# Kernel tuning notes

Measured on AMD Instinct MI355X. Metric: run time of the kernel, lower is better.

The kernel has to match this reference:

```python
import jax, jax.numpy as jnp
import numpy as np

B, N, E, H = 4, 2048, 512, 8
D = E // H  # head dim = 64


def setup_inputs() -> dict:
    key = jax.random.key(0)
    ks = jax.random.split(key, 5)
    s = 1.0 / np.sqrt(E)
    return {
        "x": jax.random.normal(ks[0], (B, N, E), dtype=jnp.float32),
        "Wk": jax.random.normal(ks[1], (E, E), dtype=jnp.float32) * s,
        "bk": jax.random.normal(ks[2], (E,), dtype=jnp.float32) * s,
        "Wv": jax.random.normal(ks[3], (E, E), dtype=jnp.float32) * s,
        "bv": jax.random.normal(ks[4], (E,), dtype=jnp.float32) * s,
    }


def reference(x, Wk, bk, Wv, bv):
    b, n, e = x.shape
    # Linear projections (torch Linear: y = x @ W.T + b), split into heads.
    keys = (x @ Wk.T + bk).reshape(b, n, H, D).transpose(0, 2, 1, 3)    # b h n d
    values = (x @ Wv.T + bv).reshape(b, n, H, D).transpose(0, 2, 1, 3)  # b h n d
    # Q = K self-attention: scores [b, h, n, n]
    dotprod = jnp.einsum('bhnd,bhmd->bhnm', keys, keys)
    # softmax over last axis, then unusual POST-softmax scaling by sqrt(emb)
    att = jax.nn.softmax(dotprod, axis=-1) / jnp.sqrt(jnp.asarray(e, x.dtype))
    # dropout p=0 -> identity
    out = jnp.einsum('bhnm,bhmd->bhnd', att, values)
    return out.transpose(0, 2, 1, 3).reshape(b, n, e)
```

## Files before the change

kernel.cpp:

```cpp
#include <hip/hip_runtime.h>

typedef __bf16 bf16_t;
typedef bf16_t bf16x8 __attribute__((ext_vector_type(8)));
typedef float f32x4 __attribute__((ext_vector_type(4)));

#define NSEQ 2048
#define EMB 512
#define HEADS 8
#define HD 64
#define BATCH 4
#define LOG2E 1.4426950408889634f

#define MFMA16(a, b, c) __builtin_amdgcn_mfma_f32_16x16x32_bf16(a, b, c, 0, 0, 0)


__global__ __launch_bounds__(256, 2) void proj_kernel(
    const float* __restrict__ x,
    const float* __restrict__ Wk, const float* __restrict__ bk,
    const float* __restrict__ Wv, const float* __restrict__ bv,
    bf16_t* __restrict__ Kf, bf16_t* __restrict__ Vf)
{
  __shared__ union {
    struct {
      __align__(16) bf16_t A[2][128][40];
      __align__(16) bf16_t B[2][128][40];
    } s;
    __align__(16) bf16_t T[128][136];
  } u;

  const int t    = threadIdx.x;
  const int w    = t >> 6;
  const int lane = t & 63;
  const int quad = lane >> 4;
  const int l15  = lane & 15;
  const int wr   = w >> 1, wc = w & 1;
  const int m0   = blockIdx.x * 128;
  const int n0   = blockIdx.y * 128;
  const int zz   = (blockIdx.y >= 4);
  const float* __restrict__ W = zz ? Wv : Wk;
  const int nW = n0 - zz * 512;

  const int sr = t >> 3;
  const int sj = t & 7;
  const int sb = sj >> 2, sc = (sj & 3) * 8;

  float4 pa[4][2], pb[4][2];
  auto prefetch = [&](int k0) {
#pragma unroll
    for (int i = 0; i < 4; ++i) {
      const float* xa = x + (size_t)(m0 + sr + i * 32) * EMB + k0 + sj * 8;
      const float* wa = W + (size_t)(nW + sr + i * 32) * EMB + k0 + sj * 8;
      pa[i][0] = *(const float4*)xa; pa[i][1] = *(const float4*)(xa + 4);
      pb[i][0] = *(const float4*)wa; pb[i][1] = *(const float4*)(wa + 4);
    }
  };
  auto pack8 = [](float4 a, float4 b) -> bf16x8 {
    bf16x8 v;
    v[0] = (bf16_t)a.x; v[1] = (bf16_t)a.y; v[2] = (bf16_t)a.z; v[3] = (bf16_t)a.w;
    v[4] = (bf16_t)b.x; v[5] = (bf16_t)b.y; v[6] = (bf16_t)b.z; v[7] = (bf16_t)b.w;
    return v;
  };

  f32x4 acc[4][4] = {};
  prefetch(0);

  for (int it = 0; it < 8; ++it) {
    __syncthreads();
#pragma unroll
    for (int i = 0; i < 4; ++i) {
      *(bf16x8*)(&u.s.A[sb][sr + i * 32][sc]) = pack8(pa[i][0], pa[i][1]);
      *(bf16x8*)(&u.s.B[sb][sr + i * 32][sc]) = pack8(pb[i][0], pb[i][1]);
    }
    __syncthreads();
    if (it < 7) prefetch((it + 1) * 64);

    bf16x8 af[4][2], bf[4][2];
#pragma unroll
    for (int mt = 0; mt < 4; ++mt)
#pragma unroll
      for (int kk = 0; kk < 2; ++kk)
        af[mt][kk] = *(const bf16x8*)(&u.s.A[kk][wr * 64 + mt * 16 + l15][quad * 8]);
#pragma unroll
    for (int nt = 0; nt < 4; ++nt)
#pragma unroll
      for (int kk = 0; kk < 2; ++kk)
        bf[nt][kk] = *(const bf16x8*)(&u.s.B[kk][wc * 64 + nt * 16 + l15][quad * 8]);
#pragma unroll
    for (int kk = 0; kk < 2; ++kk)
#pragma unroll
      for (int mt = 0; mt < 4; ++mt)
#pragma unroll
        for (int nt = 0; nt < 4; ++nt)
          acc[mt][nt] = MFMA16(af[mt][kk], bf[nt][kk], acc[mt][nt]);
  }

  __syncthreads();

#pragma unroll
  for (int mt = 0; mt < 4; ++mt) {
#pragma unroll
    for (int nt = 0; nt < 4; ++nt) {
      const int F = wc * 64 + nt * 16 + l15;
      const int c = n0 + F;
      const float bb = zz ? bv[c - 512] : bk[c];
#pragma unroll
      for (int reg = 0; reg < 4; ++reg) {
        const int R = wr * 64 + mt * 16 + quad * 4 + reg;
        const float v = acc[mt][nt][reg] + bb;
        if (!zz) u.T[R][F] = (bf16_t)v;
        else     u.T[F][R] = (bf16_t)v;
      }
    }
  }
  __syncthreads();

  if (!zz) {
#pragma unroll
    for (int i = 0; i < 8; ++i) {
      const int fi  = i * 4 + w;
      const int hL  = fi >> 4, kk = (fi >> 3) & 1, ktl = fi & 7;
      const bf16x8 v = *(const bf16x8*)(&u.T[ktl * 16 + l15][hL * 64 + kk * 32 + quad * 8]);
      const int gr = m0 + ktl * 16 + l15;
      const int b = gr >> 11, n = gr & (NSEQ - 1);
      const int bh = b * HEADS + (n0 >> 6) + hL;
      bf16_t* dst = Kf + (((size_t)(bh * 128 + (n >> 4)) * 2 + kk)) * 512 + lane * 8;
      *(bf16x8*)dst = v;
    }
  } else {
#pragma unroll
    for (int i = 0; i < 8; ++i) {
      const int fi   = i * 4 + w;
      const int hL   = fi >> 4, dt = (fi >> 2) & 3, k32l = fi & 3;
      const bf16x8 v = *(const bf16x8*)(&u.T[hL * 64 + dt * 16 + l15][k32l * 32 + quad * 8]);
      const int gr = m0 + k32l * 32;
      const int b = gr >> 11, n = gr & (NSEQ - 1);
      const int bh = b * HEADS + ((n0 - 512) >> 6) + hL;
      bf16_t* dst = Vf + (((size_t)(bh * 64 + (n >> 5)) * 4 + dt)) * 512 + lane * 8;
      *(bf16x8*)dst = v;
    }
  }
}

__global__ __launch_bounds__(256, 2) void flash_kernel(
    const bf16_t* __restrict__ Kf, const bf16_t* __restrict__ Vf,
    float* __restrict__ out)
{
  __shared__ union {
    __align__(16) bf16_t Pl[4][64][40];
    struct {
      __align__(16) float Cb[2][4096];
      __align__(16) float Lb[2][64][16];
    } c;
  } u;

  const int t    = threadIdx.x;
  const int w    = t >> 6;
  const int lane = t & 63;
  const int quad = lane >> 4;
  const int l15  = lane & 15;
  const int rh   = w & 1;
  const int kh   = w >> 1;

  const int bh = blockIdx.x;
  const int b  = bh >> 3, h = bh & 7;
  const int rowbase = blockIdx.y * 128 + rh * 64;
  const int qtile   = rowbase >> 4;

  const bf16_t* __restrict__ Kb = Kf + (size_t)bh * 128 * 2 * 512;
  const bf16_t* __restrict__ Vb = Vf + (size_t)bh * 64 * 4 * 512;

  bf16x8 qf[4][2];
#pragma unroll
  for (int nt = 0; nt < 4; ++nt)
#pragma unroll
    for (int kk = 0; kk < 2; ++kk)
      qf[nt][kk] = *(const bf16x8*)(Kb + ((size_t)(qtile + nt) * 2 + kk) * 512 + lane * 8);

  float mlog[4];
#pragma unroll
  for (int nt = 0; nt < 4; ++nt) {
    float ss = 0.f;
#pragma unroll
    for (int kk = 0; kk < 2; ++kk)
#pragma unroll
      for (int j = 0; j < 8; ++j) {
        const float qv = (float)qf[nt][kk][j];
        ss = fmaf(qv, qv, ss);
      }
    ss += __shfl_xor(ss, 16, 64);
    ss += __shfl_xor(ss, 32, 64);
    mlog[nt] = ss * LOG2E;
  }

  bf16x8 ones;
#pragma unroll
  for (int j = 0; j < 8; ++j) ones[j] = (bf16_t)1.0f;

  f32x4 acco[4][4] = {};
  f32x4 accll[4]   = {};

  auto load_k = [&](int kt, bf16x8 (&dst)[2][2]) {
    const int kb = kt * 4 + kh * 2;
#pragma unroll
    for (int jt = 0; jt < 2; ++jt)
#pragma unroll
      for (int kk = 0; kk < 2; ++kk)
        dst[jt][kk] =
            *(const bf16x8*)(Kb + ((size_t)(kb + jt) * 2 + kk) * 512 + lane * 8);
  };

  auto body = [&](int kt, bf16x8 (&kcur)[2][2], bf16x8 (&knxt)[2][2]) {
    bf16x8 vf[4];
    const int v32 = kt * 2 + kh;
#pragma unroll
    for (int dt = 0; dt < 4; ++dt)
      vf[dt] = *(const bf16x8*)(Vb + ((size_t)v32 * 4 + dt) * 512 + lane * 8);

    f32x4 st[2][4] = {};
#pragma unroll
    for (int kk = 0; kk < 2; ++kk)
#pragma unroll
      for (int jt = 0; jt < 2; ++jt)
#pragma unroll
        for (int nt = 0; nt < 4; ++nt)
          st[jt][nt] = MFMA16(kcur[jt][kk], qf[nt][kk], st[jt][nt]);

    load_k(kt + 1 < NSEQ / 64 ? kt + 1 : kt, knxt);

#pragma unroll
    for (int jt = 0; jt < 2; ++jt)
#pragma unroll
      for (int nt = 0; nt < 4; ++nt) {
        union { bf16_t hx[4]; uint2 u2; } pw;
#pragma unroll
        for (int reg = 0; reg < 4; ++reg) {
          const float p =
              __builtin_amdgcn_exp2f(fmaf(st[jt][nt][reg], LOG2E, -mlog[nt]));
          pw.hx[reg] = (bf16_t)p;
        }
        *(uint2*)(&u.Pl[w][nt * 16 + l15][jt * 16 + quad * 4]) = pw.u2;
      }

    bf16x8 pf[4];
#pragma unroll
    for (int rt = 0; rt < 4; ++rt)
      pf[rt] = *(const bf16x8*)(&u.Pl[w][rt * 16 + l15][quad * 8]);
#pragma unroll
    for (int rt = 0; rt < 4; ++rt) {
      accll[rt] = MFMA16(pf[rt], ones, accll[rt]);
#pragma unroll
      for (int dt = 0; dt < 4; ++dt)
        acco[rt][dt] = MFMA16(pf[rt], vf[dt], acco[rt][dt]);
    }
  };

  bf16x8 kA[2][2], kB[2][2];
  load_k(0, kA);
  for (int kt = 0; kt < NSEQ / 64; kt += 2) {
    body(kt,     kA, kB);
    body(kt + 1, kB, kA);
  }

  __syncthreads();
  if (kh == 1) {
#pragma unroll
    for (int rt = 0; rt < 4; ++rt) {
#pragma unroll
      for (int dt = 0; dt < 4; ++dt)
        *(f32x4*)(&u.c.Cb[rh][((rt * 4 + dt) * 64 + lane) * 4]) = acco[rt][dt];
      *(f32x4*)(&u.c.Lb[rh][lane][rt * 4]) = accll[rt];
    }
  }
  __syncthreads();
  if (kh == 0) {
#pragma unroll
    for (int rt = 0; rt < 4; ++rt) {
#pragma unroll
      for (int dt = 0; dt < 4; ++dt)
        acco[rt][dt] += *(const f32x4*)(&u.c.Cb[rh][((rt * 4 + dt) * 64 + lane) * 4]);
      accll[rt] += *(const f32x4*)(&u.c.Lb[rh][lane][rt * 4]);
    }

    const float SCL = 0.044194173824159216f;
#pragma unroll
    for (int rt = 0; rt < 4; ++rt)
#pragma unroll
      for (int reg = 0; reg < 4; ++reg) {
        const float f = SCL / accll[rt][reg];
        const int n = rowbase + rt * 16 + quad * 4 + reg;
#pragma unroll
        for (int dt = 0; dt < 4; ++dt)
          out[((size_t)(b * NSEQ + n)) * EMB + h * HD + dt * 16 + l15] =
              acco[rt][dt][reg] * f;
      }
  }
}

extern "C" void kernel_launch(void* const* d_in, const int* in_sizes, int n_in,
                              void* d_out, int out_size, void* d_ws, size_t ws_size,
                              hipStream_t stream) {
  const float* x  = (const float*)d_in[0];
  const float* Wk = (const float*)d_in[1];
  const float* bk = (const float*)d_in[2];
  const float* Wv = (const float*)d_in[3];
  const float* bv = (const float*)d_in[4];
  float* out = (float*)d_out;

  bf16_t* Kf = (bf16_t*)d_ws;
  bf16_t* Vf = Kf + (size_t)BATCH * HEADS * NSEQ * HD;

  dim3 pg(8192 / 128, 1024 / 128);
  proj_kernel<<<pg, 256, 0, stream>>>(x, Wk, bk, Wv, bv, Kf, Vf);

  dim3 fg(BATCH * HEADS, NSEQ / 128);
  flash_kernel<<<fg, 256, 0, stream>>>(Kf, Vf, out);
}
```

Before: 131.1 us.

## Build P operand in registers via permlane32 swap instead of LDS round trip

The softmax probabilities are no longer written to and reread from shared memory. Each lane packs its exp results and uses permlane32_swap to assemble the bf16x8 A-operand for the PV MFMA directly in registers. The V projection layout in proj_kernel is reordered to match the new k-ordering of P. MFMA regions are also wrapped with s_setprio to favour matrix issue. This removes LDS traffic and the write/read dependency per tile, but it relies on the element permutation being consistent across both kernels.

```diff
diff --git a/kernel.cpp b/kernel.cpp
--- a/kernel.cpp
+++ b/kernel.cpp
@@ -131,12 +131,16 @@
     for (int i = 0; i < 8; ++i) {
       const int fi   = i * 4 + w;
       const int hL   = fi >> 4, dt = (fi >> 2) & 3, k32l = fi & 3;
-      const bf16x8 v = *(const bf16x8*)(&u.T[hL * 64 + dt * 16 + l15][k32l * 32 + quad * 8]);
+      const bf16_t* Trow = &u.T[hL * 64 + dt * 16 + l15][0];
+      const int r0 = k32l * 32 + (quad >> 1) * 16 + (quad & 1) * 4;
+      union { uint2 d2[2]; bf16x8 v; } vv;
+      vv.d2[0] = *(const uint2*)(Trow + r0);
+      vv.d2[1] = *(const uint2*)(Trow + r0 + 8);
       const int gr = m0 + k32l * 32;
       const int b = gr >> 11, n = gr & (NSEQ - 1);
       const int bh = b * HEADS + ((n0 - 512) >> 6) + hL;
       bf16_t* dst = Vf + (((size_t)(bh * 64 + (n >> 5)) * 4 + dt)) * 512 + lane * 8;
-      *(bf16x8*)dst = v;
+      *(bf16x8*)dst = vv.v;
     }
   }
 }
@@ -145,12 +149,9 @@
     const bf16_t* __restrict__ Kf, const bf16_t* __restrict__ Vf,
     float* __restrict__ out)
 {
-  __shared__ union {
-    __align__(16) bf16_t Pl[4][64][40];
-    struct {
-      __align__(16) float Cb[2][4096];
-      __align__(16) float Lb[2][64][16];
-    } c;
+  __shared__ struct {
+    __align__(16) float Cb[2][4096];
+    __align__(16) float Lb[2][64][16];
   } u;
 
   const int t    = threadIdx.x;
@@ -217,6 +218,7 @@
       vf[dt] = *(const bf16x8*)(Vb + ((size_t)v32 * 4 + dt) * 512 + lane * 8);
 
     f32x4 st[2][4] = {};
+    __builtin_amdgcn_s_setprio(1);
 #pragma unroll
     for (int kk = 0; kk < 2; ++kk)
 #pragma unroll
@@ -224,27 +226,30 @@
 #pragma unroll
         for (int nt = 0; nt < 4; ++nt)
           st[jt][nt] = MFMA16(kcur[jt][kk], qf[nt][kk], st[jt][nt]);
+    __builtin_amdgcn_s_setprio(0);
 
     load_k(kt + 1 < NSEQ / 64 ? kt + 1 : kt, knxt);
 
-#pragma unroll
-    for (int jt = 0; jt < 2; ++jt)
-#pragma unroll
-      for (int nt = 0; nt < 4; ++nt) {
-        union { bf16_t hx[4]; uint2 u2; } pw;
-#pragma unroll
-        for (int reg = 0; reg < 4; ++reg) {
-          const float p =
-              __builtin_amdgcn_exp2f(fmaf(st[jt][nt][reg], LOG2E, -mlog[nt]));
-          pw.hx[reg] = (bf16_t)p;
-        }
-        *(uint2*)(&u.Pl[w][nt * 16 + l15][jt * 16 + quad * 4]) = pw.u2;
-      }
-
     bf16x8 pf[4];
 #pragma unroll
-    for (int rt = 0; rt < 4; ++rt)
-      pf[rt] = *(const bf16x8*)(&u.Pl[w][rt * 16 + l15][quad * 8]);
+    for (int nt = 0; nt < 4; ++nt) {
+      union { bf16_t h[2]; unsigned uu; } w00, w01, w10, w11;
+      w00.h[0] = (bf16_t)__builtin_amdgcn_exp2f(fmaf(st[0][nt][0], LOG2E, -mlog[nt]));
+      w00.h[1] = (bf16_t)__builtin_amdgcn_exp2f(fmaf(st[0][nt][1], LOG2E, -mlog[nt]));
+      w01.h[0] = (bf16_t)__builtin_amdgcn_exp2f(fmaf(st[0][nt][2], LOG2E, -mlog[nt]));
+      w01.h[1] = (bf16_t)__builtin_amdgcn_exp2f(fmaf(st[0][nt][3], LOG2E, -mlog[nt]));
+      w10.h[0] = (bf16_t)__builtin_amdgcn_exp2f(fmaf(st[1][nt][0], LOG2E, -mlog[nt]));
+      w10.h[1] = (bf16_t)__builtin_amdgcn_exp2f(fmaf(st[1][nt][1], LOG2E, -mlog[nt]));
+      w11.h[0] = (bf16_t)__builtin_amdgcn_exp2f(fmaf(st[1][nt][2], LOG2E, -mlog[nt]));
+      w11.h[1] = (bf16_t)__builtin_amdgcn_exp2f(fmaf(st[1][nt][3], LOG2E, -mlog[nt]));
+      auto r0 = __builtin_amdgcn_permlane32_swap(w00.uu, w10.uu, false, false);
+      auto r1 = __builtin_amdgcn_permlane32_swap(w01.uu, w11.uu, false, false);
+      union { unsigned uw[4]; bf16x8 v; } pk;
+      pk.uw[0] = r0[0]; pk.uw[1] = r1[0]; pk.uw[2] = r0[1]; pk.uw[3] = r1[1];
+      pf[nt] = pk.v;
+    }
+
+    __builtin_amdgcn_s_setprio(1);
 #pragma unroll
     for (int rt = 0; rt < 4; ++rt) {
       accll[rt] = MFMA16(pf[rt], ones, accll[rt]);
@@ -252,6 +257,7 @@
       for (int dt = 0; dt < 4; ++dt)
         acco[rt][dt] = MFMA16(pf[rt], vf[dt], acco[rt][dt]);
     }
+    __builtin_amdgcn_s_setprio(0);
   };
 
   bf16x8 kA[2][2], kB[2][2];
@@ -267,8 +273,8 @@
     for (int rt = 0; rt < 4; ++rt) {
 #pragma unroll
       for (int dt = 0; dt < 4; ++dt)
-        *(f32x4*)(&u.c.Cb[rh][((rt * 4 + dt) * 64 + lane) * 4]) = acco[rt][dt];
-      *(f32x4*)(&u.c.Lb[rh][lane][rt * 4]) = accll[rt];
+        *(f32x4*)(&u.Cb[rh][((rt * 4 + dt) * 64 + lane) * 4]) = acco[rt][dt];
+      *(f32x4*)(&u.Lb[rh][lane][rt * 4]) = accll[rt];
     }
   }
   __syncthreads();
@@ -277,8 +283,8 @@
     for (int rt = 0; rt < 4; ++rt) {
 #pragma unroll
       for (int dt = 0; dt < 4; ++dt)
-        acco[rt][dt] += *(const f32x4*)(&u.c.Cb[rh][((rt * 4 + dt) * 64 + lane) * 4]);
-      accll[rt] += *(const f32x4*)(&u.c.Lb[rh][lane][rt * 4]);
+        acco[rt][dt] += *(const f32x4*)(&u.Cb[rh][((rt * 4 + dt) * 64 + lane) * 4]);
+      accll[rt] += *(const f32x4*)(&u.Lb[rh][lane][rt * 4]);
     }
 
     const float SCL = 0.044194173824159216f;
```

Measured after the change: 129.2 us, median of 2. About the same (-1.5%).
